# Kernel tuning notes

Hardware: AMD Instinct MI355X
Metric: run time of the kernel (lower is better)

## Reference

```python
import jax, jax.numpy as jnp
import numpy as np

N = 50000        # nodes
E = 800000       # edges (avg degree 16)
D_IN = 128
HID = 128
K = 3


def cheb_edge_weights(row, col, n):
    # PyG ChebConv sym normalization with assumed lambda_max = 2.0:
    # L_hat = (2/lambda_max) * (I - D^-1/2 A D^-1/2) - I = -D^-1/2 A D^-1/2 (zero diagonal)
    mask = (row != col).astype(jnp.float32)  # remove_self_loops
    deg = jax.ops.segment_sum(mask, row, num_segments=n)
    dinv = jnp.where(deg > 0.0, jax.lax.rsqrt(jnp.maximum(deg, 1.0)), 0.0)
    return -dinv[row] * dinv[col] * mask  # [E]


def cheb_conv(x, row, col, w_edge, W, b, n):
    # Chebyshev recursion: Tx0=x, Tx1=L_hat x, Tx_k = 2 L_hat Tx_{k-1} - Tx_{k-2}
    def prop(h):  # sparse L_hat @ h via gather + segment_sum
        return jax.ops.segment_sum(w_edge[:, None] * h[col], row, num_segments=n)

    Tx0 = x
    out = Tx0 @ W[0]
    Tx1 = prop(Tx0)
    out = out + Tx1 @ W[1]
    for k in range(2, W.shape[0]):
        Tx2 = 2.0 * prop(Tx1) - Tx0
        out = out + Tx2 @ W[k]
        Tx0, Tx1 = Tx1, Tx2
    return out + b


def setup_inputs() -> dict:
    key = jax.random.key(0)
    ks = jax.random.split(key, 8)
    x = jax.random.normal(ks[0], (N, D_IN), dtype=jnp.float32)
    ei = jax.random.randint(ks[1], (2, E), 0, N, dtype=jnp.int32)
    s = 0.05
    W1 = jax.random.normal(ks[2], (K, D_IN, HID), dtype=jnp.float32) * s
    b1 = jnp.zeros((HID,), dtype=jnp.float32)
    W2 = jax.random.normal(ks[3], (K, HID, HID), dtype=jnp.float32) * s
    b2 = jnp.zeros((HID,), dtype=jnp.float32)
    W3 = jax.random.normal(ks[4], (K, HID, HID), dtype=jnp.float32) * s
    b3 = jnp.zeros((HID,), dtype=jnp.float32)
    return {"x": x, "ei": ei, "W1": W1, "b1": b1, "W2": W2, "b2": b2, "W3": W3, "b3": b3}


def reference(x, ei, W1, b1, W2, b2, W3, b3):
    row, col = ei[0], ei[1]
    w_edge = cheb_edge_weights(row, col, N)
    # layer chain: ChebConv -> ReLU -> dropout (eval mode: identity)
    h = jax.nn.relu(cheb_conv(x, row, col, w_edge, W1, b1, N))
    h = jax.nn.relu(cheb_conv(h, row, col, w_edge, W2, b2, N))
    h = jax.nn.relu(cheb_conv(h, row, col, w_edge, W3, b3, N))
    return h
```

## Files before the change

### kernel.cpp

```cpp
#include <hip/hip_runtime.h>
#include <hip/hip_bf16.h>

#define DFEAT 128

typedef short bf16x8 __attribute__((ext_vector_type(8)));
typedef float f32x4  __attribute__((ext_vector_type(4)));
typedef unsigned short u16x8 __attribute__((ext_vector_type(8)));

__device__ __forceinline__ unsigned bf16r(float f) {
    unsigned u = __float_as_uint(f);
    u += 0x7fffu + ((u >> 16) & 1u);
    return u >> 16;
}
__device__ __forceinline__ unsigned pack_bf16(float lo, float hi) {
    return bf16r(lo) | (bf16r(hi) << 16);
}
__device__ __forceinline__ float blo(unsigned v) { return __uint_as_float(v << 16); }
__device__ __forceinline__ float bhi(unsigned v) { return __uint_as_float(v & 0xffff0000u); }
__device__ __forceinline__ float f16w(unsigned cw) {
    unsigned short wb = (unsigned short)(cw >> 16);
    _Float16 hf; __builtin_memcpy(&hf, &wb, 2);
    return (float)hf;
}


__global__ void conv_kernel(const float2* __restrict__ x, unsigned* __restrict__ xb, int npk,
                            const float* __restrict__ W1, const float* __restrict__ W2,
                            const float* __restrict__ W3, unsigned short* __restrict__ Wt,
                            int* __restrict__ deg8, int N) {
    int id = blockIdx.x * blockDim.x + threadIdx.x;
    int gstride = gridDim.x * blockDim.x;
    for (int i = id; i < 8 * N; i += gstride) deg8[i] = 0;
    if (id < npk) {
        float2 v = x[id];
        xb[id] = pack_bf16(v.x, v.y);
        return;
    }
    int id2 = id - npk;
    const int PER = 3 * DFEAT * DFEAT;
    if (id2 < 3 * PER) {
        int layer = id2 / PER;
        int rem = id2 - layer * PER;
        const float* W = (layer == 0) ? W1 : ((layer == 1) ? W2 : W3);
        int seg = rem >> 14;
        int k   = (rem >> 7) & 127;
        int nn  = rem & 127;
        float w = W[rem];
        if (seg == 0) w -= W[rem + 2 * DFEAT * DFEAT];
        else if (seg == 2) w *= 2.f;
        Wt[layer * PER + (seg << 14) + (nn << 7) + k] = (unsigned short)bf16r(w);
    }
}

__global__ void deg_kernel(const int* __restrict__ ei, int* __restrict__ deg8, int E, int N) {
    int e = blockIdx.x * blockDim.x + threadIdx.x;
    if (e < E) {
        int r = ei[e];
        int c = ei[E + e];
        if (r != c) atomicAdd(&deg8[(blockIdx.x & 7) * N + r], 1);
    }
}

__global__ __launch_bounds__(1024) void scan1_kernel(const int* __restrict__ deg8,
                                                     int* __restrict__ poff,
                                                     int* __restrict__ row_ptr,
                                                     int* __restrict__ bsum,
                                                     float* __restrict__ dinv, int n) {
    __shared__ int wsums[16];
    int t = threadIdx.x;
    int idx = blockIdx.x * 1024 + t;
    int tot = 0;
    if (idx < n) {
        int run = 0;
        #pragma unroll
        for (int p = 0; p < 8; ++p) {
            int d = deg8[p * n + idx];
            poff[p * n + idx] = run;
            run += d;
        }
        tot = run;
        dinv[idx] = (tot > 0) ? rsqrtf((float)tot) : 0.f;
    }
    int vi = tot;
    #pragma unroll
    for (int off = 1; off < 64; off <<= 1) {
        int x = __shfl_up(vi, off);
        if ((t & 63) >= off) vi += x;
    }
    if ((t & 63) == 63) wsums[t >> 6] = vi;
    __syncthreads();
    if (t < 16) {
        int s = wsums[t];
        int si = s;
        #pragma unroll
        for (int off = 1; off < 16; off <<= 1) {
            int x = __shfl_up(si, off);
            if (t >= off) si += x;
        }
        wsums[t] = si - s;
        if (t == 15) bsum[blockIdx.x] = si;
    }
    __syncthreads();
    if (idx < n) row_ptr[idx + 1] = wsums[t >> 6] + vi;
}

__global__ void scan2_kernel(int* __restrict__ bsum, int nb) {
    int t = threadIdx.x;
    int carry = 0;
    for (int base = 0; base < nb; base += 64) {
        int v = (base + t < nb) ? bsum[base + t] : 0;
        int vi = v;
        #pragma unroll
        for (int off = 1; off < 64; off <<= 1) {
            int x = __shfl_up(vi, off);
            if (t >= off) vi += x;
        }
        if (base + t < nb) bsum[base + t] = carry + vi - v;
        carry += __shfl(vi, 63);
    }
}

__global__ __launch_bounds__(1024) void scan3_kernel(int* __restrict__ row_ptr,
                                                     const int* __restrict__ bsum, int n) {
    int idx = blockIdx.x * 1024 + threadIdx.x;
    if (idx == 0) row_ptr[0] = 0;
    if (idx < n) row_ptr[idx + 1] += bsum[blockIdx.x];
}

__global__ void fill_kernel(const int* __restrict__ ei, const int* __restrict__ row_ptr,
                            int* __restrict__ poff, const float* __restrict__ dinv,
                            unsigned* __restrict__ e_cw, int E, int N) {
    int e = blockIdx.x * blockDim.x + threadIdx.x;
    if (e < E) {
        int r = ei[e];
        int c = ei[E + e];
        if (r != c) {
            int p = blockIdx.x & 7;
            int k = atomicAdd(&poff[p * N + r], 1);
            int pos = row_ptr[r] + k;
            float w = -dinv[r] * dinv[c];
            _Float16 hf = (_Float16)w;
            unsigned short wb;
            __builtin_memcpy(&wb, &hf, 2);
            e_cw[pos] = (unsigned)c | ((unsigned)wb << 16);
        }
    }
}

__global__ __launch_bounds__(256) void prop_bf16_kernel(
    const uint2* __restrict__ hin2, uint2* __restrict__ hout2,
    const int* __restrict__ row_ptr, const unsigned* __restrict__ e_cw, int n)
{
    int wv = __builtin_amdgcn_readfirstlane(threadIdx.x >> 6);
    int node = blockIdx.x * 4 + wv;
    if (node >= n) return;
    const int lane = threadIdx.x & 63;
    const int h = lane >> 5;
    const int s = lane & 31;
    int rs = row_ptr[node];
    int re = row_ptr[node + 1];

    float a0 = 0.f, a1 = 0.f, a2 = 0.f, a3 = 0.f;

    for (int j = rs; j < re; j += 24) {
        uint2 vv[12]; float wv2[12];
        #pragma unroll
        for (int u = 0; u < 12; ++u) {
            int i0 = j + 2 * u;
            unsigned cw0 = (i0     < re) ? e_cw[i0]     : 0u;
            unsigned cw1 = (i0 + 1 < re) ? e_cw[i0 + 1] : 0u;
            unsigned cw = h ? cw1 : cw0;
            wv2[u] = f16w(cw);
            vv[u] = hin2[(size_t)(cw & 0xffffu) * 32 + s];
        }
        #pragma unroll
        for (int u = 0; u < 12; ++u) {
            float w = wv2[u];
            a0 += w * blo(vv[u].x);  a1 += w * bhi(vv[u].x);
            a2 += w * blo(vv[u].y);  a3 += w * bhi(vv[u].y);
        }
    }
    a0 += __shfl_xor(a0, 32);
    a1 += __shfl_xor(a1, 32);
    a2 += __shfl_xor(a2, 32);
    a3 += __shfl_xor(a3, 32);

    if (h == 0) {
        uint2 o;
        o.x = pack_bf16(a0, a1);
        o.y = pack_bf16(a2, a3);
        hout2[(size_t)node * 32 + s] = o;
    }
}

#define WPAD 136
__global__ __launch_bounds__(256) void gemm3_mfma_kernel(
    const unsigned short* __restrict__ X0, const unsigned short* __restrict__ X1,
    const unsigned short* __restrict__ X2,
    const unsigned short* __restrict__ Wt, const float* __restrict__ bias,
    void* __restrict__ out, int n, int out_bf16)
{
    __shared__ unsigned short Ws[DFEAT * WPAD];
    const int t    = threadIdx.x;
    const int wave = t >> 6;
    const int lane = t & 63;
    const int quad = lane >> 4;
    const int l16  = lane & 15;

    const int row_base = blockIdx.x * 128 + wave * 32;
    int r0 = row_base + l16;       if (r0 >= n) r0 = n - 1;
    int r1 = row_base + 16 + l16;  if (r1 >= n) r1 = n - 1;

    const unsigned short* Xps[3] = {X0, X1, X2};

    f32x4 acc[2][8];
    #pragma unroll
    for (int tt = 0; tt < 2; ++tt)
        #pragma unroll
        for (int c = 0; c < 8; ++c) acc[tt][c] = (f32x4){0.f, 0.f, 0.f, 0.f};

    const int srow = t >> 1;
    const int shalf = (t & 1) * 64;

    #pragma unroll
    for (int seg = 0; seg < 3; ++seg) {
        __syncthreads();
        const unsigned short* Wp = Wt + (seg << 14);
        #pragma unroll
        for (int i = 0; i < 8; ++i) {
            *(u16x8*)&Ws[srow * WPAD + shalf + i * 8] =
                *(const u16x8*)&Wp[srow * DFEAT + shalf + i * 8];
        }
        __syncthreads();
        const unsigned short* A0 = Xps[seg] + (size_t)r0 * DFEAT;
        const unsigned short* A1 = Xps[seg] + (size_t)r1 * DFEAT;
        #pragma unroll
        for (int kk = 0; kk < 4; ++kk) {
            const int ko = kk * 32 + quad * 8;
            bf16x8 a0 = *(const bf16x8*)(A0 + ko);
            bf16x8 a1 = *(const bf16x8*)(A1 + ko);
            #pragma unroll
            for (int c = 0; c < 8; ++c) {
                bf16x8 b = *(const bf16x8*)&Ws[(c * 16 + l16) * WPAD + ko];
                acc[0][c] = __builtin_amdgcn_mfma_f32_16x16x32_bf16(a0, b, acc[0][c], 0, 0, 0);
                acc[1][c] = __builtin_amdgcn_mfma_f32_16x16x32_bf16(a1, b, acc[1][c], 0, 0, 0);
            }
        }
    }

    #pragma unroll
    for (int tt = 0; tt < 2; ++tt) {
        int orow0 = blockIdx.x * 128 + wave * 32 + tt * 16 + quad * 4;
        #pragma unroll
        for (int c = 0; c < 8; ++c) {
            int col = c * 16 + l16;
            float bv = bias[col];
            #pragma unroll
            for (int r = 0; r < 4; ++r) {
                int orow = orow0 + r;
                if (orow < n) {
                    float v = fmaxf(acc[tt][c][r] + bv, 0.f);
                    if (out_bf16)
                        ((unsigned short*)out)[(size_t)orow * DFEAT + col] = (unsigned short)bf16r(v);
                    else
                        ((float*)out)[(size_t)orow * DFEAT + col] = v;
                }
            }
        }
    }
}

extern "C" void kernel_launch(void* const* d_in, const int* in_sizes, int n_in,
                              void* d_out, int out_size, void* d_ws, size_t ws_size,
                              hipStream_t stream) {
    const float* x  = (const float*)d_in[0];
    const int*   ei = (const int*)d_in[1];
    const float* W1 = (const float*)d_in[2];
    const float* b1 = (const float*)d_in[3];
    const float* W2 = (const float*)d_in[4];
    const float* b2 = (const float*)d_in[5];
    const float* W3 = (const float*)d_in[6];
    const float* b3 = (const float*)d_in[7];

    const int N = in_sizes[0] / DFEAT;
    const int E = in_sizes[1] / 2;
    const int NPK = N * (DFEAT / 2);
    const int NB = (N + 1023) / 1024;

    unsigned* xb  = (unsigned*)d_ws;
    unsigned* t1b = xb  + NPK;
    unsigned* t2b = t1b + NPK;
    unsigned* ab  = t2b + NPK;
    unsigned short* wt = (unsigned short*)(ab + NPK);
    int*   deg8    = (int*)(wt + 3 * 3 * DFEAT * DFEAT);
    int*   poff    = deg8 + 8 * N;
    int*   row_ptr = poff + 8 * N;
    float* dinv    = (float*)(row_ptr + (N + 2));
    unsigned* e_cw = (unsigned*)(dinv + N);
    int*   bsum    = (int*)(e_cw + E);

    const int WELEM = 3 * DFEAT * DFEAT;
    const int CONVT = NPK + 3 * WELEM;
    conv_kernel<<<(CONVT + 255) / 256, 256, 0, stream>>>(
        (const float2*)x, xb, NPK, W1, W2, W3, wt, deg8, N);
    deg_kernel<<<(E + 255) / 256, 256, 0, stream>>>(ei, deg8, E, N);
    scan1_kernel<<<NB, 1024, 0, stream>>>(deg8, poff, row_ptr, bsum, dinv, N);
    scan2_kernel<<<1, 64, 0, stream>>>(bsum, NB);
    scan3_kernel<<<NB, 1024, 0, stream>>>(row_ptr, bsum, N);
    fill_kernel<<<(E + 255) / 256, 256, 0, stream>>>(ei, row_ptr, poff, dinv, e_cw, E, N);

    const float* bl[3] = {b1, b2, b3};
    const unsigned* hin = xb;
    const int prop_grid = (N + 3) / 4;
    const int gemm_grid = (N + 127) / 128;
    for (int l = 0; l < 3; ++l) {
        prop_bf16_kernel<<<prop_grid, 256, 0, stream>>>(
            (const uint2*)hin, (uint2*)t1b, row_ptr, e_cw, N);
        prop_bf16_kernel<<<prop_grid, 256, 0, stream>>>(
            (const uint2*)t1b, (uint2*)t2b, row_ptr, e_cw, N);
        void* hout = (l == 2) ? d_out : (void*)ab;
        gemm3_mfma_kernel<<<gemm_grid, 256, 0, stream>>>(
            (const unsigned short*)hin, (const unsigned short*)t1b, (const unsigned short*)t2b,
            wt + l * WELEM, bl[l], hout, N, (l == 2) ? 0 : 1);
        hin = ab;
    }
}
```

Baseline: 389.3 us.

## Fuse second Chebyshev propagation into GEMM via LDS; merge scan passes

The second sparse propagation of each layer is now computed inside the GEMM kernel. Each wave gathers neighbour rows for 16 nodes and writes the Tx2 tile into XOR-swizzled shared memory, which the MFMA loop then reads directly. This removes one kernel launch per layer and the global write and re-read of the t2 buffer. Weights are now read straight from global memory instead of being staged in LDS. The cost is much less parallelism in the latency-bound gather: fewer waves, each walking 16 nodes one after another. The separate single-block scan2 kernel is also removed: each scan3 block sums the preceding block totals itself.

After: 489.2 us. +25.6%, slower.

```diff
diff --git a/kernel.cpp b/kernel.cpp
--- a/kernel.cpp
+++ b/kernel.cpp
@@ -104,27 +104,21 @@
     if (idx < n) row_ptr[idx + 1] = wsums[t >> 6] + vi;
 }
 
-__global__ void scan2_kernel(int* __restrict__ bsum, int nb) {
-    int t = threadIdx.x;
-    int carry = 0;
-    for (int base = 0; base < nb; base += 64) {
-        int v = (base + t < nb) ? bsum[base + t] : 0;
-        int vi = v;
-        #pragma unroll
-        for (int off = 1; off < 64; off <<= 1) {
-            int x = __shfl_up(vi, off);
-            if (t >= off) vi += x;
-        }
-        if (base + t < nb) bsum[base + t] = carry + vi - v;
-        carry += __shfl(vi, 63);
-    }
-}
-
 __global__ __launch_bounds__(1024) void scan3_kernel(int* __restrict__ row_ptr,
                                                      const int* __restrict__ bsum, int n) {
-    int idx = blockIdx.x * 1024 + threadIdx.x;
+    __shared__ int soff;
+    int t = threadIdx.x;
+    if (t < 64) {
+        int v = 0;
+        for (int k = t; k < (int)blockIdx.x; k += 64) v += bsum[k];
+        #pragma unroll
+        for (int off = 32; off > 0; off >>= 1) v += __shfl_down(v, off);
+        if (t == 0) soff = v;
+    }
+    __syncthreads();
+    int idx = blockIdx.x * 1024 + t;
     if (idx == 0) row_ptr[0] = 0;
-    if (idx < n) row_ptr[idx + 1] += bsum[blockIdx.x];
+    if (idx < n) row_ptr[idx + 1] += soff;
 }
 
 __global__ void fill_kernel(const int* __restrict__ ei, const int* __restrict__ row_ptr,
@@ -193,78 +187,115 @@
     }
 }
 
-#define WPAD 136
-__global__ __launch_bounds__(256) void gemm3_mfma_kernel(
+__global__ __launch_bounds__(256) void gemm_fused_kernel(
     const unsigned short* __restrict__ X0, const unsigned short* __restrict__ X1,
-    const unsigned short* __restrict__ X2,
     const unsigned short* __restrict__ Wt, const float* __restrict__ bias,
-    void* __restrict__ out, int n, int out_bf16)
+    void* __restrict__ out, const int* __restrict__ row_ptr,
+    const unsigned* __restrict__ e_cw, int n, int out_bf16)
 {
-    __shared__ unsigned short Ws[DFEAT * WPAD];
+    __shared__ unsigned short X2s[64 * DFEAT];
+
     const int t    = threadIdx.x;
-    const int wave = t >> 6;
+    const int wave = __builtin_amdgcn_readfirstlane(t >> 6);
     const int lane = t & 63;
+    const int row_base = blockIdx.x * 64;
+
+    {
+        const uint2* __restrict__ x1_2 = (const uint2*)X1;
+        const int h = lane >> 5;
+        const int s = lane & 31;
+        for (int i = 0; i < 16; ++i) {
+            const int lrow = wave * 16 + i;
+            const int node = row_base + lrow;
+            if (node >= n) break;
+            int rs = row_ptr[node];
+            int re = row_ptr[node + 1];
+            float a0 = 0.f, a1 = 0.f, a2 = 0.f, a3 = 0.f;
+            for (int j = rs; j < re; j += 24) {
+                uint2 vv[12]; float wv2[12];
+                #pragma unroll
+                for (int u = 0; u < 12; ++u) {
+                    int i0 = j + 2 * u;
+                    unsigned cw0 = (i0     < re) ? e_cw[i0]     : 0u;
+                    unsigned cw1 = (i0 + 1 < re) ? e_cw[i0 + 1] : 0u;
+                    unsigned cw = h ? cw1 : cw0;
+                    wv2[u] = f16w(cw);
+                    vv[u] = x1_2[(size_t)(cw & 0xffffu) * 32 + s];
+                }
+                #pragma unroll
+                for (int u = 0; u < 12; ++u) {
+                    float w = wv2[u];
+                    a0 += w * blo(vv[u].x);  a1 += w * bhi(vv[u].x);
+                    a2 += w * blo(vv[u].y);  a3 += w * bhi(vv[u].y);
+                }
+            }
+            a0 += __shfl_xor(a0, 32);
+            a1 += __shfl_xor(a1, 32);
+            a2 += __shfl_xor(a2, 32);
+            a3 += __shfl_xor(a3, 32);
+            if (h == 0) {
+                uint2 o;
+                o.x = pack_bf16(a0, a1);
+                o.y = pack_bf16(a2, a3);
+                unsigned byte = (unsigned)(lrow * 256 + s * 8);
+                byte ^= (unsigned)((lrow & 7) << 4);
+                *(uint2*)((char*)X2s + byte) = o;
+            }
+        }
+    }
+    __syncthreads();
+
     const int quad = lane >> 4;
     const int l16  = lane & 15;
-
-    const int row_base = blockIdx.x * 128 + wave * 32;
-    int r0 = row_base + l16;       if (r0 >= n) r0 = n - 1;
-    int r1 = row_base + 16 + l16;  if (r1 >= n) r1 = n - 1;
-
-    const unsigned short* Xps[3] = {X0, X1, X2};
-
-    f32x4 acc[2][8];
+    int r0 = row_base + wave * 16 + l16;
+    if (r0 >= n) r0 = n - 1;
+
+    f32x4 acc[8];
     #pragma unroll
-    for (int tt = 0; tt < 2; ++tt)
-        #pragma unroll
-        for (int c = 0; c < 8; ++c) acc[tt][c] = (f32x4){0.f, 0.f, 0.f, 0.f};
-
-    const int srow = t >> 1;
-    const int shalf = (t & 1) * 64;
+    for (int c = 0; c < 8; ++c) acc[c] = (f32x4){0.f, 0.f, 0.f, 0.f};
 
     #pragma unroll
     for (int seg = 0; seg < 3; ++seg) {
-        __syncthreads();
-        const unsigned short* Wp = Wt + (seg << 14);
-        #pragma unroll
-        for (int i = 0; i < 8; ++i) {
-            *(u16x8*)&Ws[srow * WPAD + shalf + i * 8] =
-                *(const u16x8*)&Wp[srow * DFEAT + shalf + i * 8];
-        }
-        __syncthreads();
-        const unsigned short* A0 = Xps[seg] + (size_t)r0 * DFEAT;
-        const unsigned short* A1 = Xps[seg] + (size_t)r1 * DFEAT;
-        #pragma unroll
-        for (int kk = 0; kk < 4; ++kk) {
-            const int ko = kk * 32 + quad * 8;
-            bf16x8 a0 = *(const bf16x8*)(A0 + ko);
-            bf16x8 a1 = *(const bf16x8*)(A1 + ko);
+        bf16x8 a[4];
+        if (seg < 2) {
+            const unsigned short* Ap =
+                ((seg == 0) ? X0 : X1) + (size_t)r0 * DFEAT + quad * 8;
             #pragma unroll
-            for (int c = 0; c < 8; ++c) {
-                bf16x8 b = *(const bf16x8*)&Ws[(c * 16 + l16) * WPAD + ko];
-                acc[0][c] = __builtin_amdgcn_mfma_f32_16x16x32_bf16(a0, b, acc[0][c], 0, 0, 0);
-                acc[1][c] = __builtin_amdgcn_mfma_f32_16x16x32_bf16(a1, b, acc[1][c], 0, 0, 0);
-            }
-        }
-    }
-
+            for (int kk = 0; kk < 4; ++kk) a[kk] = *(const bf16x8*)(Ap + kk * 32);
+        } else {
+            const int lr = wave * 16 + l16;
+            #pragma unroll
+            for (int kk = 0; kk < 4; ++kk) {
+                unsigned byte = (unsigned)(lr * 256 + kk * 64 + quad * 16);
+                byte ^= (unsigned)((lr & 7) << 4);
+                a[kk] = *(const bf16x8*)((const char*)X2s + byte);
+            }
+        }
+        const unsigned short* Bp = Wt + (seg << 14) + l16 * DFEAT + quad * 8;
+        #pragma unroll
+        for (int c = 0; c < 8; ++c) {
+            #pragma unroll
+            for (int kk = 0; kk < 4; ++kk) {
+                bf16x8 b = *(const bf16x8*)(Bp + c * 16 * DFEAT + kk * 32);
+                acc[c] = __builtin_amdgcn_mfma_f32_16x16x32_bf16(a[kk], b, acc[c], 0, 0, 0);
+            }
+        }
+    }
+
+    const int orow0 = row_base + wave * 16 + quad * 4;
     #pragma unroll
-    for (int tt = 0; tt < 2; ++tt) {
-        int orow0 = blockIdx.x * 128 + wave * 32 + tt * 16 + quad * 4;
-        #pragma unroll
-        for (int c = 0; c < 8; ++c) {
-            int col = c * 16 + l16;
-            float bv = bias[col];
-            #pragma unroll
-            for (int r = 0; r < 4; ++r) {
-                int orow = orow0 + r;
-                if (orow < n) {
-                    float v = fmaxf(acc[tt][c][r] + bv, 0.f);
-                    if (out_bf16)
-                        ((unsigned short*)out)[(size_t)orow * DFEAT + col] = (unsigned short)bf16r(v);
-                    else
-                        ((float*)out)[(size_t)orow * DFEAT + col] = v;
-                }
+    for (int c = 0; c < 8; ++c) {
+        const int col = c * 16 + l16;
+        const float bv = bias[col];
+        #pragma unroll
+        for (int r = 0; r < 4; ++r) {
+            const int orow = orow0 + r;
+            if (orow < n) {
+                float v = fmaxf(acc[c][r] + bv, 0.f);
+                if (out_bf16)
+                    ((unsigned short*)out)[(size_t)orow * DFEAT + col] = (unsigned short)bf16r(v);
+                else
+                    ((float*)out)[(size_t)orow * DFEAT + col] = v;
             }
         }
     }
@@ -305,23 +336,20 @@
         (const float2*)x, xb, NPK, W1, W2, W3, wt, deg8, N);
     deg_kernel<<<(E + 255) / 256, 256, 0, stream>>>(ei, deg8, E, N);
     scan1_kernel<<<NB, 1024, 0, stream>>>(deg8, poff, row_ptr, bsum, dinv, N);
-    scan2_kernel<<<1, 64, 0, stream>>>(bsum, NB);
     scan3_kernel<<<NB, 1024, 0, stream>>>(row_ptr, bsum, N);
     fill_kernel<<<(E + 255) / 256, 256, 0, stream>>>(ei, row_ptr, poff, dinv, e_cw, E, N);
 
     const float* bl[3] = {b1, b2, b3};
     const unsigned* hin = xb;
     const int prop_grid = (N + 3) / 4;
-    const int gemm_grid = (N + 127) / 128;
+    const int fused_grid = (N + 63) / 64;
     for (int l = 0; l < 3; ++l) {
         prop_bf16_kernel<<<prop_grid, 256, 0, stream>>>(
             (const uint2*)hin, (uint2*)t1b, row_ptr, e_cw, N);
-        prop_bf16_kernel<<<prop_grid, 256, 0, stream>>>(
-            (const uint2*)t1b, (uint2*)t2b, row_ptr, e_cw, N);
         void* hout = (l == 2) ? d_out : (void*)ab;
-        gemm3_mfma_kernel<<<gemm_grid, 256, 0, stream>>>(
-            (const unsigned short*)hin, (const unsigned short*)t1b, (const unsigned short*)t2b,
-            wt + l * WELEM, bl[l], hout, N, (l == 2) ? 0 : 1);
+        gemm_fused_kernel<<<fused_grid, 256, 0, stream>>>(
+            (const unsigned short*)hin, (const unsigned short*)t1b,
+            wt + l * WELEM, bl[l], hout, row_ptr, e_cw, N, (l == 2) ? 0 : 1);
         hin = ab;
     }
 }
```

## Process two nodes per wave in SpMM and fold block-sum scan into scan3

Applied to the files above, without the earlier changes.

The sparse propagation kernel now assigns two consecutive nodes to each wavefront and interleaves their gather loops, so twice as many independent row loads are in flight per wave. The grid is halved to match. Separately, the single-block scan2 launch is removed: each scan3 block sums the preceding block totals itself with a wave reduction. Risks are higher register pressure from doubled gather buffers (lower occupancy) and wasted iterations when the two nodes have unequal degree.

Measured after the change: 419.7 us. +7.8%, slower.

```diff
diff --git a/kernel.cpp b/kernel.cpp
--- a/kernel.cpp
+++ b/kernel.cpp
@@ -104,27 +104,21 @@
     if (idx < n) row_ptr[idx + 1] = wsums[t >> 6] + vi;
 }
 
-__global__ void scan2_kernel(int* __restrict__ bsum, int nb) {
-    int t = threadIdx.x;
-    int carry = 0;
-    for (int base = 0; base < nb; base += 64) {
-        int v = (base + t < nb) ? bsum[base + t] : 0;
-        int vi = v;
-        #pragma unroll
-        for (int off = 1; off < 64; off <<= 1) {
-            int x = __shfl_up(vi, off);
-            if (t >= off) vi += x;
-        }
-        if (base + t < nb) bsum[base + t] = carry + vi - v;
-        carry += __shfl(vi, 63);
-    }
-}
-
 __global__ __launch_bounds__(1024) void scan3_kernel(int* __restrict__ row_ptr,
                                                      const int* __restrict__ bsum, int n) {
-    int idx = blockIdx.x * 1024 + threadIdx.x;
+    __shared__ int soff;
+    int t = threadIdx.x;
+    if (t < 64) {
+        int v = 0;
+        for (int k = t; k < (int)blockIdx.x; k += 64) v += bsum[k];
+        #pragma unroll
+        for (int off = 32; off > 0; off >>= 1) v += __shfl_down(v, off);
+        if (t == 0) soff = v;
+    }
+    __syncthreads();
+    int idx = blockIdx.x * 1024 + t;
     if (idx == 0) row_ptr[0] = 0;
-    if (idx < n) row_ptr[idx + 1] += bsum[blockIdx.x];
+    if (idx < n) row_ptr[idx + 1] += soff;
 }
 
 __global__ void fill_kernel(const int* __restrict__ ei, const int* __restrict__ row_ptr,
@@ -152,44 +146,78 @@
     const int* __restrict__ row_ptr, const unsigned* __restrict__ e_cw, int n)
 {
     int wv = __builtin_amdgcn_readfirstlane(threadIdx.x >> 6);
-    int node = blockIdx.x * 4 + wv;
-    if (node >= n) return;
+    int nodeA = blockIdx.x * 8 + wv * 2;
+    if (nodeA >= n) return;
+    const int nodeB = nodeA + 1;
+    const bool hasB = nodeB < n;
     const int lane = threadIdx.x & 63;
     const int h = lane >> 5;
     const int s = lane & 31;
-    int rs = row_ptr[node];
-    int re = row_ptr[node + 1];
-
-    float a0 = 0.f, a1 = 0.f, a2 = 0.f, a3 = 0.f;
-
-    for (int j = rs; j < re; j += 24) {
-        uint2 vv[12]; float wv2[12];
+
+    int rsA = row_ptr[nodeA];
+    int reA = row_ptr[nodeA + 1];
+    int reB = hasB ? row_ptr[nodeB + 1] : reA;
+
+    float aA0 = 0.f, aA1 = 0.f, aA2 = 0.f, aA3 = 0.f;
+    float aB0 = 0.f, aB1 = 0.f, aB2 = 0.f, aB3 = 0.f;
+
+    int jA = rsA, jB = reA;
+    while (jA < reA || jB < reB) {
+        uint2 vA[12]; float wA[12];
+        uint2 vB[12]; float wB[12];
         #pragma unroll
         for (int u = 0; u < 12; ++u) {
-            int i0 = j + 2 * u;
-            unsigned cw0 = (i0     < re) ? e_cw[i0]     : 0u;
-            unsigned cw1 = (i0 + 1 < re) ? e_cw[i0 + 1] : 0u;
+            int i0 = jA + 2 * u;
+            unsigned cw0 = (i0     < reA) ? e_cw[i0]     : 0u;
+            unsigned cw1 = (i0 + 1 < reA) ? e_cw[i0 + 1] : 0u;
             unsigned cw = h ? cw1 : cw0;
-            wv2[u] = f16w(cw);
-            vv[u] = hin2[(size_t)(cw & 0xffffu) * 32 + s];
+            wA[u] = f16w(cw);
+            vA[u] = hin2[(size_t)(cw & 0xffffu) * 32 + s];
         }
         #pragma unroll
         for (int u = 0; u < 12; ++u) {
-            float w = wv2[u];
-            a0 += w * blo(vv[u].x);  a1 += w * bhi(vv[u].x);
-            a2 += w * blo(vv[u].y);  a3 += w * bhi(vv[u].y);
-        }
-    }
-    a0 += __shfl_xor(a0, 32);
-    a1 += __shfl_xor(a1, 32);
-    a2 += __shfl_xor(a2, 32);
-    a3 += __shfl_xor(a3, 32);
+            int i0 = jB + 2 * u;
+            unsigned cw0 = (i0     < reB) ? e_cw[i0]     : 0u;
+            unsigned cw1 = (i0 + 1 < reB) ? e_cw[i0 + 1] : 0u;
+            unsigned cw = h ? cw1 : cw0;
+            wB[u] = f16w(cw);
+            vB[u] = hin2[(size_t)(cw & 0xffffu) * 32 + s];
+        }
+        #pragma unroll
+        for (int u = 0; u < 12; ++u) {
+            float w = wA[u];
+            aA0 += w * blo(vA[u].x);  aA1 += w * bhi(vA[u].x);
+            aA2 += w * blo(vA[u].y);  aA3 += w * bhi(vA[u].y);
+        }
+        #pragma unroll
+        for (int u = 0; u < 12; ++u) {
+            float w = wB[u];
+            aB0 += w * blo(vB[u].x);  aB1 += w * bhi(vB[u].x);
+            aB2 += w * blo(vB[u].y);  aB3 += w * bhi(vB[u].y);
+        }
+        jA += 24; jB += 24;
+    }
+
+    aA0 += __shfl_xor(aA0, 32);
+    aA1 += __shfl_xor(aA1, 32);
+    aA2 += __shfl_xor(aA2, 32);
+    aA3 += __shfl_xor(aA3, 32);
+    aB0 += __shfl_xor(aB0, 32);
+    aB1 += __shfl_xor(aB1, 32);
+    aB2 += __shfl_xor(aB2, 32);
+    aB3 += __shfl_xor(aB3, 32);
 
     if (h == 0) {
         uint2 o;
-        o.x = pack_bf16(a0, a1);
-        o.y = pack_bf16(a2, a3);
-        hout2[(size_t)node * 32 + s] = o;
+        o.x = pack_bf16(aA0, aA1);
+        o.y = pack_bf16(aA2, aA3);
+        hout2[(size_t)nodeA * 32 + s] = o;
+        if (hasB) {
+            uint2 o2;
+            o2.x = pack_bf16(aB0, aB1);
+            o2.y = pack_bf16(aB2, aB3);
+            hout2[(size_t)nodeB * 32 + s] = o2;
+        }
     }
 }
 
@@ -305,13 +333,12 @@
         (const float2*)x, xb, NPK, W1, W2, W3, wt, deg8, N);
     deg_kernel<<<(E + 255) / 256, 256, 0, stream>>>(ei, deg8, E, N);
     scan1_kernel<<<NB, 1024, 0, stream>>>(deg8, poff, row_ptr, bsum, dinv, N);
-    scan2_kernel<<<1, 64, 0, stream>>>(bsum, NB);
     scan3_kernel<<<NB, 1024, 0, stream>>>(row_ptr, bsum, N);
     fill_kernel<<<(E + 255) / 256, 256, 0, stream>>>(ei, row_ptr, poff, dinv, e_cw, E, N);
 
     const float* bl[3] = {b1, b2, b3};
     const unsigned* hin = xb;
-    const int prop_grid = (N + 3) / 4;
+    const int prop_grid = (N + 7) / 8;
     const int gemm_grid = (N + 127) / 128;
     for (int l = 0; l < 3; ++l) {
         prop_bf16_kernel<<<prop_grid, 256, 0, stream>>>(
```

## Switch activations to fp16 with packed half2 accumulation and fuse scan passes

Applied to the files above, without the earlier changes.

Converts the stored activations and weights from bf16 to fp16, and uses the fp16 MFMA in the GEMM. The gather-propagate kernel now accumulates with packed half2 FMAs instead of unpacking to fp32, cutting the conversion and FMA instruction count in the memory-bound inner loop. Separately, the single-block scan2 pass is removed: each scan3 block sums the preceding block totals itself, saving one launch. The fp16 accumulation risks precision loss and overflow, since the range is narrower than bf16 and the sums stay in half precision.

Measured after the change: 388.4 us. About the same (-0.3%).

```diff
diff --git a/kernel.cpp b/kernel.cpp
--- a/kernel.cpp
+++ b/kernel.cpp
@@ -3,25 +3,21 @@
 
 #define DFEAT 128
 
-typedef short bf16x8 __attribute__((ext_vector_type(8)));
+typedef _Float16 h2 __attribute__((ext_vector_type(2)));
+typedef _Float16 f16x8 __attribute__((ext_vector_type(8)));
 typedef float f32x4  __attribute__((ext_vector_type(4)));
 typedef unsigned short u16x8 __attribute__((ext_vector_type(8)));
 
-__device__ __forceinline__ unsigned bf16r(float f) {
-    unsigned u = __float_as_uint(f);
-    u += 0x7fffu + ((u >> 16) & 1u);
-    return u >> 16;
-}
-__device__ __forceinline__ unsigned pack_bf16(float lo, float hi) {
-    return bf16r(lo) | (bf16r(hi) << 16);
-}
-__device__ __forceinline__ float blo(unsigned v) { return __uint_as_float(v << 16); }
-__device__ __forceinline__ float bhi(unsigned v) { return __uint_as_float(v & 0xffff0000u); }
-__device__ __forceinline__ float f16w(unsigned cw) {
-    unsigned short wb = (unsigned short)(cw >> 16);
-    _Float16 hf; __builtin_memcpy(&hf, &wb, 2);
-    return (float)hf;
-}
+__device__ __forceinline__ unsigned short f16b(float f) {
+    _Float16 hf = (_Float16)f;
+    unsigned short b; __builtin_memcpy(&b, &hf, 2);
+    return b;
+}
+__device__ __forceinline__ unsigned pack_f16(float lo, float hi) {
+    return (unsigned)f16b(lo) | ((unsigned)f16b(hi) << 16);
+}
+__device__ __forceinline__ float h2f(h2 v) { float f; __builtin_memcpy(&f, &v, 4); return f; }
+__device__ __forceinline__ h2 f2h(float f) { h2 v; __builtin_memcpy(&v, &f, 4); return v; }
 
 
 __global__ void conv_kernel(const float2* __restrict__ x, unsigned* __restrict__ xb, int npk,
@@ -33,7 +29,7 @@
     for (int i = id; i < 8 * N; i += gstride) deg8[i] = 0;
     if (id < npk) {
         float2 v = x[id];
-        xb[id] = pack_bf16(v.x, v.y);
+        xb[id] = pack_f16(v.x, v.y);
         return;
     }
     int id2 = id - npk;
@@ -48,7 +44,7 @@
         float w = W[rem];
         if (seg == 0) w -= W[rem + 2 * DFEAT * DFEAT];
         else if (seg == 2) w *= 2.f;
-        Wt[layer * PER + (seg << 14) + (nn << 7) + k] = (unsigned short)bf16r(w);
+        Wt[layer * PER + (seg << 14) + (nn << 7) + k] = f16b(w);
     }
 }
 
@@ -104,27 +100,21 @@
     if (idx < n) row_ptr[idx + 1] = wsums[t >> 6] + vi;
 }
 
-__global__ void scan2_kernel(int* __restrict__ bsum, int nb) {
-    int t = threadIdx.x;
-    int carry = 0;
-    for (int base = 0; base < nb; base += 64) {
-        int v = (base + t < nb) ? bsum[base + t] : 0;
-        int vi = v;
-        #pragma unroll
-        for (int off = 1; off < 64; off <<= 1) {
-            int x = __shfl_up(vi, off);
-            if (t >= off) vi += x;
-        }
-        if (base + t < nb) bsum[base + t] = carry + vi - v;
-        carry += __shfl(vi, 63);
-    }
-}
-
 __global__ __launch_bounds__(1024) void scan3_kernel(int* __restrict__ row_ptr,
                                                      const int* __restrict__ bsum, int n) {
-    int idx = blockIdx.x * 1024 + threadIdx.x;
+    __shared__ int soff;
+    int t = threadIdx.x;
+    if (t < 64) {
+        int v = 0;
+        for (int k = t; k < (int)blockIdx.x; k += 64) v += bsum[k];
+        #pragma unroll
+        for (int off = 32; off > 0; off >>= 1) v += __shfl_down(v, off);
+        if (t == 0) soff = v;
+    }
+    __syncthreads();
+    int idx = blockIdx.x * 1024 + t;
     if (idx == 0) row_ptr[0] = 0;
-    if (idx < n) row_ptr[idx + 1] += bsum[blockIdx.x];
+    if (idx < n) row_ptr[idx + 1] += soff;
 }
 
 __global__ void fill_kernel(const int* __restrict__ ei, const int* __restrict__ row_ptr,
@@ -139,15 +129,12 @@
             int k = atomicAdd(&poff[p * N + r], 1);
             int pos = row_ptr[r] + k;
             float w = -dinv[r] * dinv[c];
-            _Float16 hf = (_Float16)w;
-            unsigned short wb;
-            __builtin_memcpy(&wb, &hf, 2);
-            e_cw[pos] = (unsigned)c | ((unsigned)wb << 16);
-        }
-    }
-}
-
-__global__ __launch_bounds__(256) void prop_bf16_kernel(
+            e_cw[pos] = (unsigned)c | ((unsigned)f16b(w) << 16);
+        }
+    }
+}
+
+__global__ __launch_bounds__(256) void prop_f16_kernel(
     const uint2* __restrict__ hin2, uint2* __restrict__ hout2,
     const int* __restrict__ row_ptr, const unsigned* __restrict__ e_cw, int n)
 {
@@ -160,35 +147,34 @@
     int rs = row_ptr[node];
     int re = row_ptr[node + 1];
 
-    float a0 = 0.f, a1 = 0.f, a2 = 0.f, a3 = 0.f;
+    h2 a01 = {(_Float16)0.f, (_Float16)0.f};
+    h2 a23 = {(_Float16)0.f, (_Float16)0.f};
 
     for (int j = rs; j < re; j += 24) {
-        uint2 vv[12]; float wv2[12];
+        uint2 vv[12]; unsigned ww[12];
         #pragma unroll
         for (int u = 0; u < 12; ++u) {
             int i0 = j + 2 * u;
             unsigned cw0 = (i0     < re) ? e_cw[i0]     : 0u;
             unsigned cw1 = (i0 + 1 < re) ? e_cw[i0 + 1] : 0u;
             unsigned cw = h ? cw1 : cw0;
-            wv2[u] = f16w(cw);
+            ww[u] = (cw & 0xffff0000u) | (cw >> 16);
             vv[u] = hin2[(size_t)(cw & 0xffffu) * 32 + s];
         }
         #pragma unroll
         for (int u = 0; u < 12; ++u) {
-            float w = wv2[u];
-            a0 += w * blo(vv[u].x);  a1 += w * bhi(vv[u].x);
-            a2 += w * blo(vv[u].y);  a3 += w * bhi(vv[u].y);
-        }
-    }
-    a0 += __shfl_xor(a0, 32);
-    a1 += __shfl_xor(a1, 32);
-    a2 += __shfl_xor(a2, 32);
-    a3 += __shfl_xor(a3, 32);
+            h2 wp = f2h(__uint_as_float(ww[u]));
+            a01 = f2h(__uint_as_float(vv[u].x)) * wp + a01;
+            a23 = f2h(__uint_as_float(vv[u].y)) * wp + a23;
+        }
+    }
+    a01 = a01 + f2h(__shfl_xor(h2f(a01), 32));
+    a23 = a23 + f2h(__shfl_xor(h2f(a23), 32));
 
     if (h == 0) {
         uint2 o;
-        o.x = pack_bf16(a0, a1);
-        o.y = pack_bf16(a2, a3);
+        o.x = __float_as_uint(h2f(a01));
+        o.y = __float_as_uint(h2f(a23));
         hout2[(size_t)node * 32 + s] = o;
     }
 }
@@ -198,7 +184,7 @@
     const unsigned short* __restrict__ X0, const unsigned short* __restrict__ X1,
     const unsigned short* __restrict__ X2,
     const unsigned short* __restrict__ Wt, const float* __restrict__ bias,
-    void* __restrict__ out, int n, int out_bf16)
+    void* __restrict__ out, int n, int out_f16)
 {
     __shared__ unsigned short Ws[DFEAT * WPAD];
     const int t    = threadIdx.x;
@@ -237,13 +223,13 @@
         #pragma unroll
         for (int kk = 0; kk < 4; ++kk) {
             const int ko = kk * 32 + quad * 8;
-            bf16x8 a0 = *(const bf16x8*)(A0 + ko);
-            bf16x8 a1 = *(const bf16x8*)(A1 + ko);
+            f16x8 a0 = *(const f16x8*)(A0 + ko);
+            f16x8 a1 = *(const f16x8*)(A1 + ko);
             #pragma unroll
             for (int c = 0; c < 8; ++c) {
-                bf16x8 b = *(const bf16x8*)&Ws[(c * 16 + l16) * WPAD + ko];
-                acc[0][c] = __builtin_amdgcn_mfma_f32_16x16x32_bf16(a0, b, acc[0][c], 0, 0, 0);
-                acc[1][c] = __builtin_amdgcn_mfma_f32_16x16x32_bf16(a1, b, acc[1][c], 0, 0, 0);
+                f16x8 b = *(const f16x8*)&Ws[(c * 16 + l16) * WPAD + ko];
+                acc[0][c] = __builtin_amdgcn_mfma_f32_16x16x32_f16(a0, b, acc[0][c], 0, 0, 0);
+                acc[1][c] = __builtin_amdgcn_mfma_f32_16x16x32_f16(a1, b, acc[1][c], 0, 0, 0);
             }
         }
     }
@@ -260,8 +246,8 @@
                 int orow = orow0 + r;
                 if (orow < n) {
                     float v = fmaxf(acc[tt][c][r] + bv, 0.f);
-                    if (out_bf16)
-                        ((unsigned short*)out)[(size_t)orow * DFEAT + col] = (unsigned short)bf16r(v);
+                    if (out_f16)
+                        ((unsigned short*)out)[(size_t)orow * DFEAT + col] = f16b(v);
                     else
                         ((float*)out)[(size_t)orow * DFEAT + col] = v;
                 }
@@ -305,7 +291,6 @@
         (const float2*)x, xb, NPK, W1, W2, W3, wt, deg8, N);
     deg_kernel<<<(E + 255) / 256, 256, 0, stream>>>(ei, deg8, E, N);
     scan1_kernel<<<NB, 1024, 0, stream>>>(deg8, poff, row_ptr, bsum, dinv, N);
-    scan2_kernel<<<1, 64, 0, stream>>>(bsum, NB);
     scan3_kernel<<<NB, 1024, 0, stream>>>(row_ptr, bsum, N);
     fill_kernel<<<(E + 255) / 256, 256, 0, stream>>>(ei, row_ptr, poff, dinv, e_cw, E, N);
 
@@ -314,9 +299,9 @@
     const int prop_grid = (N + 3) / 4;
     const int gemm_grid = (N + 127) / 128;
     for (int l = 0; l < 3; ++l) {
-        prop_bf16_kernel<<<prop_grid, 256, 0, stream>>>(
+        prop_f16_kernel<<<prop_grid, 256, 0, stream>>>(
             (const uint2*)hin, (uint2*)t1b, row_ptr, e_cw, N);
-        prop_bf16_kernel<<<prop_grid, 256, 0, stream>>>(
+        prop_f16_kernel<<<prop_grid, 256, 0, stream>>>(
             (const uint2*)t1b, (uint2*)t2b, row_ptr, e_cw, N);
         void* hout = (l == 2) ? d_out : (void*)ab;
         gemm3_mfma_kernel<<<gemm_grid, 256, 0, stream>>>(
```
